# Optimization experiments

Measured on AMD Instinct MI355X. Metric: run time of the kernel, lower is better.

The kernel has to match this reference:

```python
import jax, jax.numpy as jnp
import numpy as np

B, C, H, W = 8, 64, 256, 256
EPS = 1e-5


def setup_inputs() -> dict:
    key = jax.random.key(0)
    ks = jax.random.split(key, 8)
    s = 1.0 / np.sqrt(C)
    return {
        "x": jax.random.normal(ks[0], (B, C, H, W), dtype=jnp.float32),
        "Wq": jax.random.uniform(ks[1], (C, C), jnp.float32, -s, s),
        "bq": jnp.zeros((C,), jnp.float32),
        "Wk": jax.random.uniform(ks[2], (C, C), jnp.float32, -s, s),
        "bk": jnp.zeros((C,), jnp.float32),
        "Wv": jax.random.uniform(ks[3], (C, C), jnp.float32, -s, s),
        "bv": jnp.zeros((C,), jnp.float32),
        "gamma": jnp.ones((C,), jnp.float32),
        "beta": jnp.zeros((C,), jnp.float32),
        "running_mean": jnp.zeros((C,), jnp.float32),
        "running_var": jnp.ones((C,), jnp.float32),
        "alpha": jnp.full((1,), 0.25, jnp.float32),  # PReLU single shared parameter
    }


def _conv1x1(x, w, b):
    # 1x1 conv == per-pixel channel mixing: [B,Ci,H,W] x [Co,Ci] -> [B,Co,H,W]
    return jnp.einsum("bihw,oi->bohw", x, w) + b[None, :, None, None]


def reference(x, Wq, bq, Wk, bk, Wv, bv, gamma, beta, running_mean, running_var, alpha):
    # d_k = sqrt(H); scores scaled by d_k**0.5 -> H**0.25 (faithful to source)
    scale = jnp.asarray(H, x.dtype) ** 0.25
    Q = _conv1x1(x, Wq, bq)
    K = _conv1x1(x, Wk, bk)
    V = _conv1x1(x, Wv, bv)
    # scores over spatial rows: [B,C,H,H]
    scores = jnp.einsum("bchw,bcgw->bchg", Q, K) / scale
    attn = jax.nn.softmax(scores, axis=-1)
    out = jnp.einsum("bchg,bcgw->bchw", attn, V)
    # BatchNorm2d (eval mode: running stats), then PReLU; dropout is identity in eval
    inv = gamma / jnp.sqrt(running_var + EPS)
    out = out * inv[None, :, None, None] + (beta - running_mean * inv)[None, :, None, None]
    a = alpha[0]
    out = jnp.where(out >= 0, out, a * out)
    return out
```

## Files before the change

kernel.cpp:

```cpp
#include <hip/hip_runtime.h>

#define B_ 8
#define C_ 64
#define H_ 256
#define W_ 256
#define HW_ 65536
#define PLANE_ 33554432

typedef __attribute__((ext_vector_type(8))) short short8;
typedef __attribute__((ext_vector_type(4))) float f32x4;

__device__ __forceinline__ unsigned short f2bf(float f){
  unsigned u = __float_as_uint(f);
  u += 0x7fffu + ((u >> 16) & 1u);
  return (unsigned short)(u >> 16);
}

__global__ __launch_bounds__(256) void proj_kernel(
    const float* __restrict__ x,
    const float* __restrict__ Wq, const float* __restrict__ bq,
    const float* __restrict__ Wk, const float* __restrict__ bk,
    const float* __restrict__ Wv, const float* __restrict__ bv,
    unsigned short* __restrict__ Qb, unsigned short* __restrict__ Kb,
    unsigned short* __restrict__ Vb)
{
  __shared__ unsigned short Xt[W_*64];
  __shared__ unsigned short Wl[3*64*64];
  const int tid = threadIdx.x;
  const int lane = tid & 63;
  const int wv  = tid >> 6;
  const int q4 = lane >> 4, l16 = lane & 15;
  const int bid = blockIdx.x;
  const int b = bid >> 8, h = bid & 255;

  const float* wsrc[3] = {Wq, Wk, Wv};
  #pragma unroll
  for (int p=0;p<3;++p){
    const float* wp = wsrc[p];
    for (int idx=tid; idx<4096; idx+=256){
      int o = idx >> 6, i = idx & 63;
      Wl[p*4096 + o*64 + (i ^ ((o&7)<<3))] = f2bf(wp[idx]);
    }
  }
  {
    const float* xb = x + (size_t)b*C_*HW_ + (size_t)h*W_;
    #pragma unroll
    for (int it=0; it<16; ++it){
      int i = it*4 + wv;
      float4 v = *(const float4*)(xb + (size_t)i*HW_ + lane*4);
      float fv[4] = {v.x, v.y, v.z, v.w};
      #pragma unroll
      for (int k2=0;k2<4;++k2){
        int w = lane*4 + k2;
        int slot = (w&7) ^ ((w>>3)&7);
        Xt[w*64 + (i ^ (slot<<3))] = f2bf(fv[k2]);
      }
    }
  }
  __syncthreads();

  unsigned short* outp[3] = {Qb, Kb, Vb};
  const float* bsrc[3] = {bq, bk, bv};
  const size_t obase = (size_t)b*C_*HW_ + (size_t)h*W_;

  #pragma unroll
  for (int p=0;p<3;++p){
    short8 afr[4][2];
    #pragma unroll
    for (int mf=0;mf<4;++mf){
      #pragma unroll
      for (int kk=0;kk<2;++kk){
        int o = mf*16 + l16;
        int i = (32*kk + 8*q4) ^ ((o&7)<<3);
        afr[mf][kk] = *(const short8*)&Wl[p*4096 + o*64 + i];
      }
    }
    f32x4 acc[4][4];
    #pragma unroll
    for (int mf=0;mf<4;++mf){
      #pragma unroll
      for (int nf=0;nf<4;++nf){ f32x4 z = {0.f,0.f,0.f,0.f}; acc[mf][nf] = z; }
    }
    #pragma unroll
    for (int nf=0;nf<4;++nf){
      int w = wv*64 + nf*16 + l16;
      int slot = (w&7) ^ ((w>>3)&7);
      #pragma unroll
      for (int kk=0;kk<2;++kk){
        short8 bfr = *(const short8*)&Xt[w*64 + ((32*kk + 8*q4) ^ (slot<<3))];
        #pragma unroll
        for (int mf=0;mf<4;++mf)
          acc[mf][nf] = __builtin_amdgcn_mfma_f32_16x16x32_bf16(afr[mf][kk], bfr, acc[mf][nf], 0,0,0);
      }
    }
    unsigned short* op = outp[p];
    const float* bp = bsrc[p];
    #pragma unroll
    for (int mf=0;mf<4;++mf){
      #pragma unroll
      for (int r=0;r<4;++r){
        int o = mf*16 + 4*q4 + r;
        float bias = bp[o];
        #pragma unroll
        for (int nf=0;nf<4;++nf){
          int w = wv*64 + nf*16 + l16;
          op[obase + (size_t)o*HW_ + w] = f2bf(acc[mf][nf][r] + bias);
        }
      }
    }
  }
}

__global__ __launch_bounds__(256) void transpose_v(unsigned short* __restrict__ Vb)
{
  const int pi[10] = {0,0,0,0,1,1,1,2,2,3};
  const int pj[10] = {0,1,2,3,1,2,3,2,3,3};
  __shared__ unsigned short tA[64*65];
  __shared__ unsigned short tB[64*65];
  int t = threadIdx.x;
  int bid = blockIdx.x;
  int bc = bid / 10, pr = bid - bc*10;
  int ti = pi[pr], tj = pj[pr];
  unsigned short* base = Vb + (size_t)bc*HW_;
  int diag = (ti == tj);
  #pragma unroll
  for (int k=0;k<2;++k){
    int flat = t + k*256;
    int i = flat >> 3, j = (flat & 7)*8;
    int4 va = *(const int4*)(base + (size_t)(ti*64+i)*256 + tj*64 + j);
    const unsigned short* pa = (const unsigned short*)&va;
    #pragma unroll
    for (int e=0;e<8;++e) tA[i*65 + j + e] = pa[e];
    if (!diag){
      int4 vb2 = *(const int4*)(base + (size_t)(tj*64+i)*256 + ti*64 + j);
      const unsigned short* pb = (const unsigned short*)&vb2;
      #pragma unroll
      for (int e=0;e<8;++e) tB[i*65 + j + e] = pb[e];
    }
  }
  __syncthreads();
  #pragma unroll
  for (int k=0;k<2;++k){
    int flat = t + k*256;
    int i = flat >> 3, j = (flat & 7)*8;
    int4 vo; unsigned short* po = (unsigned short*)&vo;
    #pragma unroll
    for (int e=0;e<8;++e) po[e] = tA[(j+e)*65 + i];
    *(int4*)(base + (size_t)(tj*64+i)*256 + ti*64 + j) = vo;
    if (!diag){
      int4 vo2; unsigned short* po2 = (unsigned short*)&vo2;
      #pragma unroll
      for (int e=0;e<8;++e) po2[e] = tB[(j+e)*65 + i];
      *(int4*)(base + (size_t)(ti*64+i)*256 + tj*64 + j) = vo2;
    }
  }
}

__device__ __forceinline__ void copy_tile_swz(unsigned short* dst, const unsigned short* src, int tid){
  const int4* s = (const int4*)src;
  int4* d = (int4*)dst;
  #pragma unroll
  for (int k=0;k<8;++k){
    int f = tid + k*256;
    d[f ^ ((f>>5)&7)] = s[f];
  }
}

__global__ __launch_bounds__(256) void attn_kernel(
    const unsigned short* __restrict__ Qb, const unsigned short* __restrict__ Kb,
    const unsigned short* __restrict__ Vtb,
    const float* __restrict__ gamma, const float* __restrict__ beta,
    const float* __restrict__ rmean, const float* __restrict__ rvar,
    const float* __restrict__ alphaP,
    float* __restrict__ out)
{
  __shared__ unsigned short s_q [64*256];
  __shared__ unsigned short s_kv[64*256];
  const int tid = threadIdx.x;
  const int lane = tid & 63;
  const int wv = tid >> 6;
  const int q4 = lane >> 4, l16 = lane & 15;
  const int bid = blockIdx.x;
  const int bc = bid >> 2, ht = bid & 3;
  const int c = bc & 63;

  const unsigned short* Qp = Qb  + (size_t)bc*HW_ + ht*64*W_;
  const unsigned short* Kp = Kb  + (size_t)bc*HW_;
  const unsigned short* Vp = Vtb + (size_t)bc*HW_;

  copy_tile_swz(s_q,  Qp, tid);
  copy_tile_swz(s_kv, Kp, tid);
  __syncthreads();

  short8 aq[8];
  {
    int row = wv*16 + l16;
    int sw = (row&7)<<3;
    #pragma unroll
    for (int kk=0;kk<8;++kk)
      aq[kk] = *(const short8*)&s_q[row*256 + ((8*q4 + 32*kk) ^ sw)];
  }

  f32x4 sa[16];
  #pragma unroll
  for (int f=0;f<16;++f){ f32x4 z = {0.f,0.f,0.f,0.f}; sa[f] = z; }

  #pragma unroll
  for (int gt=0; gt<4; ++gt){
    #pragma unroll
    for (int nf=0;nf<4;++nf){
      int g = nf*16 + l16;
      int sw = (g&7)<<3;
      int f = gt*4 + nf;
      #pragma unroll
      for (int kk=0;kk<8;++kk){
        short8 bf_ = *(const short8*)&s_kv[g*256 + ((8*q4 + 32*kk) ^ sw)];
        sa[f] = __builtin_amdgcn_mfma_f32_16x16x32_bf16(aq[kk], bf_, sa[f], 0,0,0);
      }
    }
    __syncthreads();
    if (gt < 3){
      copy_tile_swz(s_kv, Kp + (gt+1)*64*W_, tid);
      __syncthreads();
    }
  }

  float mrow[4], rden[4], psum[4];
  #pragma unroll
  for (int r=0;r<4;++r){
    float m = -3.0e38f;
    #pragma unroll
    for (int f=0;f<16;++f) m = fmaxf(m, sa[f][r]);
    m = fmaxf(m, __shfl_xor(m, 1, 16));
    m = fmaxf(m, __shfl_xor(m, 2, 16));
    m = fmaxf(m, __shfl_xor(m, 4, 16));
    m = fmaxf(m, __shfl_xor(m, 8, 16));
    mrow[r] = m;
    psum[r] = 0.f;
  }
  const float cs = 0.25f * 1.4426950408889634f;
  #pragma unroll
  for (int f=0;f<16;++f){
    #pragma unroll
    for (int r=0;r<4;++r){
      float pv = exp2f((sa[f][r] - mrow[r]) * cs);
      sa[f][r] = pv;
      psum[r] += pv;
    }
  }
  #pragma unroll
  for (int r=0;r<4;++r){
    float s = psum[r];
    s += __shfl_xor(s, 1, 16);
    s += __shfl_xor(s, 2, 16);
    s += __shfl_xor(s, 4, 16);
    s += __shfl_xor(s, 8, 16);
    rden[r] = 1.0f / s;
  }
  #pragma unroll
  for (int r=0;r<4;++r){
    int row = wv*16 + 4*q4 + r;
    int sw = (row&7)<<3;
    #pragma unroll
    for (int f=0;f<16;++f){
      int g = l16 + 16*f;
      s_q[row*256 + (g ^ sw)] = f2bf(sa[f][r]);
    }
  }

  short8 ap[8];
  {
    int row = wv*16 + l16;
    int sw = (row&7)<<3;
    #pragma unroll
    for (int kk=0;kk<8;++kk)
      ap[kk] = *(const short8*)&s_q[row*256 + ((8*q4 + 32*kk) ^ sw)];
  }

  f32x4 oa[16];
  #pragma unroll
  for (int f=0;f<16;++f){ f32x4 z = {0.f,0.f,0.f,0.f}; oa[f] = z; }

  #pragma unroll
  for (int wt=0; wt<4; ++wt){
    __syncthreads();
    copy_tile_swz(s_kv, Vp + wt*64*W_, tid);
    __syncthreads();
    #pragma unroll
    for (int nf=0;nf<4;++nf){
      int wl = nf*16 + l16;
      int sw = (wl&7)<<3;
      int fo = wt*4 + nf;
      #pragma unroll
      for (int kk=0;kk<8;++kk){
        short8 bf_ = *(const short8*)&s_kv[wl*256 + ((8*q4 + 32*kk) ^ sw)];
        oa[fo] = __builtin_amdgcn_mfma_f32_16x16x32_bf16(ap[kk], bf_, oa[fo], 0,0,0);
      }
    }
  }

  float inv   = gamma[c] / sqrtf(rvar[c] + 1e-5f);
  float shift = beta[c] - rmean[c]*inv;
  float al    = alphaP[0];
  float* ob = out + (size_t)bc*HW_ + ht*64*W_;
  #pragma unroll
  for (int wt=0; wt<4; ++wt){
    #pragma unroll
    for (int nf=0; nf<4; ++nf){
      int fo = wt*4 + nf;
      int w = wt*64 + nf*16 + l16;
      #pragma unroll
      for (int r=0;r<4;++r){
        int row = wv*16 + 4*q4 + r;
        float v = oa[fo][r] * rden[r];
        v = v*inv + shift;
        v = (v >= 0.f) ? v : al*v;
        ob[(size_t)row*W_ + w] = v;
      }
    }
  }
}

extern "C" void kernel_launch(void* const* d_in, const int* in_sizes, int n_in,
                              void* d_out, int out_size, void* d_ws, size_t ws_size,
                              hipStream_t stream)
{
  const float* x     = (const float*)d_in[0];
  const float* Wq    = (const float*)d_in[1];
  const float* bq    = (const float*)d_in[2];
  const float* Wk    = (const float*)d_in[3];
  const float* bk    = (const float*)d_in[4];
  const float* Wv    = (const float*)d_in[5];
  const float* bv    = (const float*)d_in[6];
  const float* gamma = (const float*)d_in[7];
  const float* beta  = (const float*)d_in[8];
  const float* rmean = (const float*)d_in[9];
  const float* rvar  = (const float*)d_in[10];
  const float* alpha = (const float*)d_in[11];
  float* out = (float*)d_out;

  unsigned short* Qb = (unsigned short*)d_ws;
  unsigned short* Kb = Qb + (size_t)PLANE_;
  unsigned short* Vb = Kb + (size_t)PLANE_;

  proj_kernel<<<B_*H_, 256, 0, stream>>>(x, Wq,bq, Wk,bk, Wv,bv, Qb, Kb, Vb);
  transpose_v<<<B_*C_*10, 256, 0, stream>>>(Vb);
  attn_kernel<<<B_*C_*4, 256, 0, stream>>>(Qb, Kb, Vb, gamma, beta, rmean, rvar, alpha, out);
}
```

Measured before the change: 396.6 us.

## Rework projection and attention kernels with direct-to-LDS loads and vectorized stores

The projection kernel drops the shared-memory weight staging and reads weights straight from global into registers, swapping operand roles so each lane writes packed 4-element bf16 stores. The transpose kernel switches to padded int4 LDS writes. The attention kernel uses a single LDS buffer filled by global_load_lds with a new swizzle, reads Q fragments directly from global, and folds the softmax normalisation into P before the second GEMM. It also swaps MFMA operand order so output stores are float4 vectors, and remaps block IDs for locality. These changes aim to cut LDS traffic and occupancy pressure and to widen global stores, at the risk of added sync points and less latency hiding.

```diff
diff --git a/kernel.cpp b/kernel.cpp
--- a/kernel.cpp
+++ b/kernel.cpp
@@ -9,6 +9,7 @@
 
 typedef __attribute__((ext_vector_type(8))) short short8;
 typedef __attribute__((ext_vector_type(4))) float f32x4;
+typedef __attribute__((ext_vector_type(4))) unsigned short ushort4v;
 
 __device__ __forceinline__ unsigned short f2bf(float f){
   unsigned u = __float_as_uint(f);
@@ -25,7 +26,6 @@
     unsigned short* __restrict__ Vb)
 {
   __shared__ unsigned short Xt[W_*64];
-  __shared__ unsigned short Wl[3*64*64];
   const int tid = threadIdx.x;
   const int lane = tid & 63;
   const int wv  = tid >> 6;
@@ -33,15 +33,6 @@
   const int bid = blockIdx.x;
   const int b = bid >> 8, h = bid & 255;
 
-  const float* wsrc[3] = {Wq, Wk, Wv};
-  #pragma unroll
-  for (int p=0;p<3;++p){
-    const float* wp = wsrc[p];
-    for (int idx=tid; idx<4096; idx+=256){
-      int o = idx >> 6, i = idx & 63;
-      Wl[p*4096 + o*64 + (i ^ ((o&7)<<3))] = f2bf(wp[idx]);
-    }
-  }
   {
     const float* xb = x + (size_t)b*C_*HW_ + (size_t)h*W_;
     #pragma unroll
@@ -59,53 +50,56 @@
   }
   __syncthreads();
 
+  short8 aX[4][2];
+  #pragma unroll
+  for (int mf=0;mf<4;++mf){
+    int w = wv*64 + mf*16 + l16;
+    int slot = (w&7) ^ ((w>>3)&7);
+    #pragma unroll
+    for (int kk=0;kk<2;++kk)
+      aX[mf][kk] = *(const short8*)&Xt[w*64 + ((8*q4 + 32*kk) ^ (slot<<3))];
+  }
+
+  const float* wsrc[3] = {Wq, Wk, Wv};
+  const float* bsrc[3] = {bq, bk, bv};
   unsigned short* outp[3] = {Qb, Kb, Vb};
-  const float* bsrc[3] = {bq, bk, bv};
   const size_t obase = (size_t)b*C_*HW_ + (size_t)h*W_;
 
   #pragma unroll
   for (int p=0;p<3;++p){
-    short8 afr[4][2];
-    #pragma unroll
-    for (int mf=0;mf<4;++mf){
+    const float* wp = wsrc[p];
+    unsigned short* op = outp[p];
+    #pragma unroll
+    for (int nf=0;nf<4;++nf){
+      const int o = nf*16 + l16;
+      const float bias = bsrc[p][o];
+      short8 bW[2];
       #pragma unroll
       for (int kk=0;kk<2;++kk){
-        int o = mf*16 + l16;
-        int i = (32*kk + 8*q4) ^ ((o&7)<<3);
-        afr[mf][kk] = *(const short8*)&Wl[p*4096 + o*64 + i];
-      }
-    }
-    f32x4 acc[4][4];
-    #pragma unroll
-    for (int mf=0;mf<4;++mf){
-      #pragma unroll
-      for (int nf=0;nf<4;++nf){ f32x4 z = {0.f,0.f,0.f,0.f}; acc[mf][nf] = z; }
-    }
-    #pragma unroll
-    for (int nf=0;nf<4;++nf){
-      int w = wv*64 + nf*16 + l16;
-      int slot = (w&7) ^ ((w>>3)&7);
-      #pragma unroll
-      for (int kk=0;kk<2;++kk){
-        short8 bfr = *(const short8*)&Xt[w*64 + ((32*kk + 8*q4) ^ (slot<<3))];
+        const float* ws = wp + o*64 + 8*q4 + 32*kk;
+        float4 w0 = *(const float4*)ws;
+        float4 w1 = *(const float4*)(ws+4);
+        short8 t;
+        t[0]=(short)f2bf(w0.x); t[1]=(short)f2bf(w0.y);
+        t[2]=(short)f2bf(w0.z); t[3]=(short)f2bf(w0.w);
+        t[4]=(short)f2bf(w1.x); t[5]=(short)f2bf(w1.y);
+        t[6]=(short)f2bf(w1.z); t[7]=(short)f2bf(w1.w);
+        bW[kk]=t;
+      }
+      f32x4 acc[4];
+      #pragma unroll
+      for (int mf=0;mf<4;++mf){ f32x4 z={0.f,0.f,0.f,0.f}; acc[mf]=z; }
+      #pragma unroll
+      for (int kk=0;kk<2;++kk)
         #pragma unroll
         for (int mf=0;mf<4;++mf)
-          acc[mf][nf] = __builtin_amdgcn_mfma_f32_16x16x32_bf16(afr[mf][kk], bfr, acc[mf][nf], 0,0,0);
-      }
-    }
-    unsigned short* op = outp[p];
-    const float* bp = bsrc[p];
-    #pragma unroll
-    for (int mf=0;mf<4;++mf){
-      #pragma unroll
-      for (int r=0;r<4;++r){
-        int o = mf*16 + 4*q4 + r;
-        float bias = bp[o];
+          acc[mf] = __builtin_amdgcn_mfma_f32_16x16x32_bf16(aX[mf][kk], bW[kk], acc[mf], 0,0,0);
+      #pragma unroll
+      for (int mf=0;mf<4;++mf){
+        ushort4v sv;
         #pragma unroll
-        for (int nf=0;nf<4;++nf){
-          int w = wv*64 + nf*16 + l16;
-          op[obase + (size_t)o*HW_ + w] = f2bf(acc[mf][nf][r] + bias);
-        }
+        for (int r=0;r<4;++r) sv[r] = f2bf(acc[mf][r] + bias);
+        *(ushort4v*)&op[obase + (size_t)o*HW_ + (wv*64 + mf*16 + 4*q4)] = sv;
       }
     }
   }
@@ -115,8 +109,8 @@
 {
   const int pi[10] = {0,0,0,0,1,1,1,2,2,3};
   const int pj[10] = {0,1,2,3,1,2,3,2,3,3};
-  __shared__ unsigned short tA[64*65];
-  __shared__ unsigned short tB[64*65];
+  __shared__ unsigned short tA[64*72];
+  __shared__ unsigned short tB[64*72];
   int t = threadIdx.x;
   int bid = blockIdx.x;
   int bc = bid / 10, pr = bid - bc*10;
@@ -128,14 +122,10 @@
     int flat = t + k*256;
     int i = flat >> 3, j = (flat & 7)*8;
     int4 va = *(const int4*)(base + (size_t)(ti*64+i)*256 + tj*64 + j);
-    const unsigned short* pa = (const unsigned short*)&va;
-    #pragma unroll
-    for (int e=0;e<8;++e) tA[i*65 + j + e] = pa[e];
+    *(int4*)&tA[i*72 + j] = va;
     if (!diag){
       int4 vb2 = *(const int4*)(base + (size_t)(tj*64+i)*256 + ti*64 + j);
-      const unsigned short* pb = (const unsigned short*)&vb2;
-      #pragma unroll
-      for (int e=0;e<8;++e) tB[i*65 + j + e] = pb[e];
+      *(int4*)&tB[i*72 + j] = vb2;
     }
   }
   __syncthreads();
@@ -145,24 +135,28 @@
     int i = flat >> 3, j = (flat & 7)*8;
     int4 vo; unsigned short* po = (unsigned short*)&vo;
     #pragma unroll
-    for (int e=0;e<8;++e) po[e] = tA[(j+e)*65 + i];
+    for (int e=0;e<8;++e) po[e] = tA[(j+e)*72 + i];
     *(int4*)(base + (size_t)(tj*64+i)*256 + ti*64 + j) = vo;
     if (!diag){
       int4 vo2; unsigned short* po2 = (unsigned short*)&vo2;
       #pragma unroll
-      for (int e=0;e<8;++e) po2[e] = tB[(j+e)*65 + i];
+      for (int e=0;e<8;++e) po2[e] = tB[(j+e)*72 + i];
       *(int4*)(base + (size_t)(ti*64+i)*256 + tj*64 + j) = vo2;
     }
   }
 }
 
-__device__ __forceinline__ void copy_tile_swz(unsigned short* dst, const unsigned short* src, int tid){
-  const int4* s = (const int4*)src;
-  int4* d = (int4*)dst;
+__device__ __forceinline__ int swzkey(int r){ return (r & 31) ^ ((r & 3) << 3); }
+
+__device__ __forceinline__ void stage_tile(unsigned short* dst, const unsigned short* src, int tid){
   #pragma unroll
   for (int k=0;k<8;++k){
-    int f = tid + k*256;
-    d[f ^ ((f>>5)&7)] = s[f];
+    int j = tid + k*256;
+    int gj = j ^ swzkey(j >> 5);
+    __builtin_amdgcn_global_load_lds(
+      (const __attribute__((address_space(1))) void*)(src + (size_t)gj*8),
+      (__attribute__((address_space(3))) void*)(dst + (size_t)j*8),
+      16, 0, 0);
   }
 }
 
@@ -174,58 +168,56 @@
     const float* __restrict__ alphaP,
     float* __restrict__ out)
 {
-  __shared__ unsigned short s_q [64*256];
-  __shared__ unsigned short s_kv[64*256];
+  __shared__ unsigned short s[64*256];
   const int tid = threadIdx.x;
   const int lane = tid & 63;
   const int wv = tid >> 6;
   const int q4 = lane >> 4, l16 = lane & 15;
-  const int bid = blockIdx.x;
-  const int bc = bid >> 2, ht = bid & 3;
+  const int n = blockIdx.x;
+  const int work = (n & 7)*256 + (n >> 3);
+  const int bc = work >> 2, ht = work & 3;
   const int c = bc & 63;
 
-  const unsigned short* Qp = Qb  + (size_t)bc*HW_ + ht*64*W_;
+  const unsigned short* Qp = Qb  + (size_t)bc*HW_ + (size_t)ht*64*W_;
   const unsigned short* Kp = Kb  + (size_t)bc*HW_;
   const unsigned short* Vp = Vtb + (size_t)bc*HW_;
 
-  copy_tile_swz(s_q,  Qp, tid);
-  copy_tile_swz(s_kv, Kp, tid);
-  __syncthreads();
+  stage_tile(s, Kp, tid);
 
   short8 aq[8];
   {
-    int row = wv*16 + l16;
-    int sw = (row&7)<<3;
+    const int row = wv*16 + l16;
     #pragma unroll
     for (int kk=0;kk<8;++kk)
-      aq[kk] = *(const short8*)&s_q[row*256 + ((8*q4 + 32*kk) ^ sw)];
+      aq[kk] = *(const short8*)(Qp + (size_t)row*W_ + 8*q4 + 32*kk);
   }
 
   f32x4 sa[16];
   #pragma unroll
-  for (int f=0;f<16;++f){ f32x4 z = {0.f,0.f,0.f,0.f}; sa[f] = z; }
-
+  for (int f=0;f<16;++f){ f32x4 z={0.f,0.f,0.f,0.f}; sa[f]=z; }
+
+  __syncthreads();
   #pragma unroll
   for (int gt=0; gt<4; ++gt){
     #pragma unroll
     for (int nf=0;nf<4;++nf){
-      int g = nf*16 + l16;
-      int sw = (g&7)<<3;
-      int f = gt*4 + nf;
+      const int g = nf*16 + l16;
+      const int ko = swzkey(g);
+      const int f = gt*4 + nf;
       #pragma unroll
       for (int kk=0;kk<8;++kk){
-        short8 bf_ = *(const short8*)&s_kv[g*256 + ((8*q4 + 32*kk) ^ sw)];
-        sa[f] = __builtin_amdgcn_mfma_f32_16x16x32_bf16(aq[kk], bf_, sa[f], 0,0,0);
+        short8 bk_ = *(const short8*)&s[g*256 + (((q4 + 4*kk) ^ ko) << 3)];
+        sa[f] = __builtin_amdgcn_mfma_f32_16x16x32_bf16(aq[kk], bk_, sa[f], 0,0,0);
       }
     }
     __syncthreads();
     if (gt < 3){
-      copy_tile_swz(s_kv, Kp + (gt+1)*64*W_, tid);
+      stage_tile(s, Kp + (size_t)(gt+1)*64*W_, tid);
       __syncthreads();
     }
   }
 
-  float mrow[4], rden[4], psum[4];
+  float mrow[4], rden[4];
   #pragma unroll
   for (int r=0;r<4;++r){
     float m = -3.0e38f;
@@ -236,9 +228,9 @@
     m = fmaxf(m, __shfl_xor(m, 4, 16));
     m = fmaxf(m, __shfl_xor(m, 8, 16));
     mrow[r] = m;
-    psum[r] = 0.f;
   }
   const float cs = 0.25f * 1.4426950408889634f;
+  float psum[4] = {0.f,0.f,0.f,0.f};
   #pragma unroll
   for (int f=0;f<16;++f){
     #pragma unroll
@@ -250,74 +242,76 @@
   }
   #pragma unroll
   for (int r=0;r<4;++r){
-    float s = psum[r];
-    s += __shfl_xor(s, 1, 16);
-    s += __shfl_xor(s, 2, 16);
-    s += __shfl_xor(s, 4, 16);
-    s += __shfl_xor(s, 8, 16);
-    rden[r] = 1.0f / s;
-  }
+    float ssum = psum[r];
+    ssum += __shfl_xor(ssum, 1, 16);
+    ssum += __shfl_xor(ssum, 2, 16);
+    ssum += __shfl_xor(ssum, 4, 16);
+    ssum += __shfl_xor(ssum, 8, 16);
+    rden[r] = 1.0f / ssum;
+  }
+
   #pragma unroll
   for (int r=0;r<4;++r){
-    int row = wv*16 + 4*q4 + r;
-    int sw = (row&7)<<3;
+    const int row = wv*16 + 4*q4 + r;
+    const int ko = swzkey(row);
     #pragma unroll
     for (int f=0;f<16;++f){
-      int g = l16 + 16*f;
-      s_q[row*256 + (g ^ sw)] = f2bf(sa[f][r]);
-    }
-  }
-
-  short8 ap[8];
+      const int g2 = l16 + 16*f;
+      s[row*256 + ((((g2>>3) ^ ko) << 3) | (g2 & 7))] = f2bf(sa[f][r] * rden[r]);
+    }
+  }
+  __syncthreads();
+
+  short8 pb[8];
   {
-    int row = wv*16 + l16;
-    int sw = (row&7)<<3;
+    const int row = wv*16 + l16;
+    const int ko = swzkey(row);
     #pragma unroll
     for (int kk=0;kk<8;++kk)
-      ap[kk] = *(const short8*)&s_q[row*256 + ((8*q4 + 32*kk) ^ sw)];
-  }
+      pb[kk] = *(const short8*)&s[row*256 + (((q4 + 4*kk) ^ ko) << 3)];
+  }
+  __syncthreads();
 
   f32x4 oa[16];
   #pragma unroll
-  for (int f=0;f<16;++f){ f32x4 z = {0.f,0.f,0.f,0.f}; oa[f] = z; }
-
+  for (int f=0;f<16;++f){ f32x4 z={0.f,0.f,0.f,0.f}; oa[f]=z; }
+
+  stage_tile(s, Vp, tid);
+  __syncthreads();
   #pragma unroll
   for (int wt=0; wt<4; ++wt){
+    #pragma unroll
+    for (int nf=0;nf<4;++nf){
+      const int wrow = nf*16 + l16;
+      const int ko = swzkey(wrow);
+      const int mw = wt*4 + nf;
+      #pragma unroll
+      for (int kk=0;kk<8;++kk){
+        short8 av = *(const short8*)&s[wrow*256 + (((q4 + 4*kk) ^ ko) << 3)];
+        oa[mw] = __builtin_amdgcn_mfma_f32_16x16x32_bf16(av, pb[kk], oa[mw], 0,0,0);
+      }
+    }
     __syncthreads();
-    copy_tile_swz(s_kv, Vp + wt*64*W_, tid);
-    __syncthreads();
-    #pragma unroll
-    for (int nf=0;nf<4;++nf){
-      int wl = nf*16 + l16;
-      int sw = (wl&7)<<3;
-      int fo = wt*4 + nf;
-      #pragma unroll
-      for (int kk=0;kk<8;++kk){
-        short8 bf_ = *(const short8*)&s_kv[wl*256 + ((8*q4 + 32*kk) ^ sw)];
-        oa[fo] = __builtin_amdgcn_mfma_f32_16x16x32_bf16(ap[kk], bf_, oa[fo], 0,0,0);
-      }
-    }
-  }
-
-  float inv   = gamma[c] / sqrtf(rvar[c] + 1e-5f);
-  float shift = beta[c] - rmean[c]*inv;
-  float al    = alphaP[0];
-  float* ob = out + (size_t)bc*HW_ + ht*64*W_;
-  #pragma unroll
-  for (int wt=0; wt<4; ++wt){
-    #pragma unroll
-    for (int nf=0; nf<4; ++nf){
-      int fo = wt*4 + nf;
-      int w = wt*64 + nf*16 + l16;
-      #pragma unroll
-      for (int r=0;r<4;++r){
-        int row = wv*16 + 4*q4 + r;
-        float v = oa[fo][r] * rden[r];
-        v = v*inv + shift;
-        v = (v >= 0.f) ? v : al*v;
-        ob[(size_t)row*W_ + w] = v;
-      }
-    }
+    if (wt < 3){
+      stage_tile(s, Vp + (size_t)(wt+1)*64*W_, tid);
+      __syncthreads();
+    }
+  }
+
+  const float inv   = gamma[c] / sqrtf(rvar[c] + 1e-5f);
+  const float shift = beta[c] - rmean[c]*inv;
+  const float al    = alphaP[0];
+  float* ob = out + (size_t)bc*HW_ + (size_t)ht*64*W_;
+  const int hrow = wv*16 + l16;
+  #pragma unroll
+  for (int mw=0; mw<16; ++mw){
+    f32x4 v;
+    #pragma unroll
+    for (int r=0;r<4;++r){
+      float t = oa[mw][r]*inv + shift;
+      v[r] = (t >= 0.f) ? t : al*t;
+    }
+    *(f32x4*)&ob[(size_t)hrow*W_ + mw*16 + 4*q4] = v;
   }
 }
 
```

Measured after the change: 430.3 us. +8.5%, slower.
